# Performance work log

Hardware: AMD Instinct MI355X
Metric: run time of the kernel (lower is better)

The kernel has to match this reference:

```python
import jax, jax.numpy as jnp
import numpy as np

B, NN, HIS, MSG = 16, 1000, 12, 64
NODE_DIM, EDGE_DIM, META_DIM = 32, 16, 128
GAT_DIM = HIS * MSG            # 768
META_IN = NODE_DIM + GAT_DIM   # 800
N = B * NN                     # 16000 total nodes
E = 128000
NEG_SLOPE = 0.2


def setup_inputs() -> dict:
    key = jax.random.key(0)
    ks = jax.random.split(key, 16)
    def glorot(k, shape):
        fan_in = shape[0]
        lim = 1.0 / np.sqrt(fan_in)
        return jax.random.uniform(k, shape, jnp.float32, -lim, lim)
    return {
        "node_feature": jax.random.normal(ks[0], (B, NN, NODE_DIM), jnp.float32),
        "edge_attr": jax.random.normal(ks[1], (E, EDGE_DIM), jnp.float32),
        "message_feature": jax.random.normal(ks[2], (B, NN, HIS, MSG), jnp.float32),
        "edge_index": jax.random.randint(ks[3], (2, E), 0, N, jnp.int64) if jax.config.jax_enable_x64 else jax.random.randint(ks[3], (2, E), 0, N, jnp.int32),
        # node_learner / edge_learner
        "W_node": glorot(ks[4], (NODE_DIM, NODE_DIM)),
        "b_node": jnp.zeros((NODE_DIM,), jnp.float32),
        "W_edge": glorot(ks[5], (EDGE_DIM, EDGE_DIM)),
        "b_edge": jnp.zeros((EDGE_DIM,), jnp.float32),
        # GATConv(768, 768, heads=1, concat=False)
        "W_gat": glorot(ks[6], (GAT_DIM, GAT_DIM)),
        "att_src": glorot(ks[7], (GAT_DIM,)) * 0.1,
        "att_dst": glorot(ks[8], (GAT_DIM,)) * 0.1,
        "b_gat": jnp.zeros((GAT_DIM,), jnp.float32),
        # GNNConv([meta_in, meta_dim], dim=edge_dim)
        "W_nbr": glorot(ks[9], (2 * META_IN + EDGE_DIM, META_DIM)),
        "b_nbr": jnp.zeros((META_DIM,), jnp.float32),
        "W_self": glorot(ks[10], (META_IN, META_DIM)),
        "b_self": jnp.zeros((META_DIM,), jnp.float32),
    }


def reference(node_feature, edge_attr, message_feature, edge_index,
              W_node, b_node, W_edge, b_edge,
              W_gat, att_src, att_dst, b_gat,
              W_nbr, b_nbr, W_self, b_self):
    src, dst = edge_index[0], edge_index[1]  # j -> i

    # node / edge learners
    nf = (node_feature @ W_node + b_node).reshape(-1, NODE_DIM)        # [N, 32]
    ea = edge_attr @ W_edge + b_edge                                   # [E, 16]
    mf = message_feature.reshape(-1, GAT_DIM)                          # [N, 768]

    # --- GATConv (1 head, concat=False, add_self_loops=True, eval: no dropout) ---
    loops = jnp.arange(N, dtype=src.dtype)
    src_sl = jnp.concatenate([src, loops])
    dst_sl = jnp.concatenate([dst, loops])
    h = mf @ W_gat                                                     # [N, 768]
    a_src = h @ att_src                                                # [N]
    a_dst = h @ att_dst                                                # [N]
    alpha = jax.nn.leaky_relu(a_src[src_sl] + a_dst[dst_sl], NEG_SLOPE)  # [E+N]
    amax = jax.ops.segment_max(alpha, dst_sl, num_segments=N)
    ex = jnp.exp(alpha - amax[dst_sl])
    denom = jax.ops.segment_sum(ex, dst_sl, num_segments=N)
    coef = ex / denom[dst_sl]
    gat_out = jax.ops.segment_sum(h[src_sl] * coef[:, None], dst_sl, num_segments=N) + b_gat

    # --- meta input + GNNConv (aggr='add', batch_norm=False) ---
    x = jnp.concatenate([gat_out, nf], axis=-1)                        # [N, 800]
    z = jnp.concatenate([x[dst], x[src], ea], axis=-1)                 # [E, 1616]
    msg = z @ W_nbr + b_nbr                                            # [E, 128]
    agg = jax.ops.segment_sum(msg, dst, num_segments=N)                # [N, 128]
    out = agg + x @ W_self + b_self                                    # [N, 128]
    return out.reshape(-1, NN, META_DIM)                               # [B, 1000, 128]
```

## Files before the change

### kernel.cpp

```cpp
#include <hip/hip_runtime.h>

#define N_NODES 16000
#define N_EDGES 128000
#define GATD 768
#define NODED 32
#define EDGED 16
#define METAIN 800
#define METAD 128
#define YCOLS 384

typedef short s16x8 __attribute__((ext_vector_type(8)));
typedef float f32x4v __attribute__((ext_vector_type(4)));

__device__ __forceinline__ unsigned short f2bf(float f){
    unsigned u = __float_as_uint(f);
    return (unsigned short)((u + 0x7fffu + ((u >> 16) & 1u)) >> 16);
}
__device__ __forceinline__ float us2f(unsigned short u){ return __uint_as_float(((unsigned)u)<<16); }

__device__ __forceinline__ void gload16(const void* g, void* l){
    __builtin_amdgcn_global_load_lds((const __attribute__((address_space(1))) void*)g,
                                     (__attribute__((address_space(3))) void*)l, 16, 0, 0);
}


__global__ __launch_bounds__(256) void conv_bf16_kernel(const float* __restrict__ in,
                                                        unsigned short* __restrict__ out, int n8){
    int i = blockIdx.x*256 + threadIdx.x;
    if (i >= n8) return;
    const float4* p = reinterpret_cast<const float4*>(in) + (size_t)i*2;
    float4 a = p[0], b = p[1];
    union { unsigned short u[8]; s16x8 v; } o;
    o.u[0]=f2bf(a.x); o.u[1]=f2bf(a.y); o.u[2]=f2bf(a.z); o.u[3]=f2bf(a.w);
    o.u[4]=f2bf(b.x); o.u[5]=f2bf(b.y); o.u[6]=f2bf(b.z); o.u[7]=f2bf(b.w);
    reinterpret_cast<s16x8*>(out)[i] = o.v;
}

__global__ __launch_bounds__(256) void wgat_t_kernel(const float* __restrict__ W_gat,
                                                     unsigned short* __restrict__ WgT){
    int idx = blockIdx.x*256 + threadIdx.x;
    int c = idx / GATD, k = idx % GATD;
    WgT[idx] = f2bf(W_gat[(size_t)k*GATD + c]);
}

__global__ __launch_bounds__(256) void wcat_t_kernel(const float* __restrict__ W_nbr,
                                                     const float* __restrict__ W_self,
                                                     unsigned short* __restrict__ WcatT){
    int idx = blockIdx.x*256 + threadIdx.x;
    int c = idx / METAIN, k = idx % METAIN;
    float v;
    if (c < 128)      v = W_nbr[(size_t)k*METAD + c];
    else if (c < 256) v = W_nbr[(size_t)(800+k)*METAD + (c-128)];
    else              v = W_self[(size_t)k*METAD + (c-256)];
    WcatT[idx] = f2bf(v);
}


__global__ __launch_bounds__(256) void ea_kernel(const float* __restrict__ edge_attr,
                                                 const float* __restrict__ W_edge,
                                                 const float* __restrict__ b_edge,
                                                 float* __restrict__ ea_lin){
    __shared__ float We[256];
    __shared__ float be[16];
    int tid = threadIdx.x;
    We[tid] = W_edge[tid];
    if (tid < 16) be[tid] = b_edge[tid];
    __syncthreads();
    int idx = blockIdx.x*256 + tid;
    int e = idx >> 4, j = idx & 15;
    const float* row = edge_attr + (size_t)e*EDGED;
    float s = be[j];
    #pragma unroll
    for (int k = 0; k < 16; ++k) s += row[k] * We[k*16 + j];
    ea_lin[idx] = s;
}

__global__ __launch_bounds__(256) void nf_kernel(const float* __restrict__ node_feature,
                                                 const float* __restrict__ W_node,
                                                 const float* __restrict__ b_node,
                                                 unsigned short* __restrict__ x_bf){
    __shared__ float Wn[1024];
    __shared__ float bn[32];
    int tid = threadIdx.x;
    for (int i = tid; i < 1024; i += 256) Wn[i] = W_node[i];
    if (tid < 32) bn[tid] = b_node[tid];
    __syncthreads();
    int idx = blockIdx.x*256 + tid;
    int n = idx >> 5, j = idx & 31;
    const float* row = node_feature + (size_t)n*NODED;
    float s = bn[j];
    #pragma unroll
    for (int k = 0; k < 32; ++k) s += row[k] * Wn[k*32 + j];
    x_bf[(size_t)n*METAIN + GATD + j] = f2bf(s);
}


__global__ __launch_bounds__(256) void deg_kernel(const int* __restrict__ dst, int* __restrict__ deg){
    int e = blockIdx.x*256 + threadIdx.x;
    atomicAdd(&deg[dst[e]], 1);
}

__global__ __launch_bounds__(1024) void scan_kernel(const int* __restrict__ deg,
                                                    int* __restrict__ rowstart,
                                                    int* __restrict__ cursor){
    __shared__ int part[1024];
    int t = threadIdx.x;
    int base = t * 16;
    int local[16];
    int s = 0;
    #pragma unroll
    for (int k = 0; k < 16; ++k){
        int idx = base + k;
        int v = (idx < N_NODES) ? deg[idx] : 0;
        local[k] = s; s += v;
    }
    part[t] = s;
    __syncthreads();
    for (int off = 1; off < 1024; off <<= 1){
        int v = 0;
        if (t >= off) v = part[t-off];
        __syncthreads();
        if (t >= off) part[t] += v;
        __syncthreads();
    }
    int excl = (t == 0) ? 0 : part[t-1];
    #pragma unroll
    for (int k = 0; k < 16; ++k){
        int idx = base + k;
        if (idx < N_NODES){ int rs = excl + local[k]; rowstart[idx] = rs; cursor[idx] = rs; }
    }
    if (t == 1023) rowstart[N_NODES] = part[1023];
}

__global__ __launch_bounds__(256) void csr_kernel(const int* __restrict__ dst,
                                                  int* __restrict__ cursor,
                                                  int* __restrict__ csr){
    int e = blockIdx.x*256 + threadIdx.x;
    int p = atomicAdd(&cursor[dst[e]], 1);
    csr[p] = e;
}


template<bool BFOUT>
__global__ __launch_bounds__(256) void mfma_gemm_kernel(const unsigned short* __restrict__ A,
                                                        const unsigned short* __restrict__ Bt,
                                                        float* __restrict__ Cf,
                                                        unsigned short* __restrict__ Cb,
                                                        int Ncols, int K){
    __shared__ __align__(16) unsigned short As[128*32];
    __shared__ __align__(16) unsigned short Bs[128*32];
    int tid = threadIdx.x;
    int wave = tid >> 6, lane = tid & 63;
    int rowBase = blockIdx.y * 128, colBase = blockIdx.x * 128;
    const unsigned short* gA = A + (size_t)(rowBase + (tid>>2))*K + (tid&3)*8;
    const unsigned short* gB = Bt + (size_t)(colBase + (tid>>2))*K + (tid&3)*8;
    char* lA = (char*)As + tid*16;
    char* lB = (char*)Bs + tid*16;
    int r0 = (wave>>1)*64, c0 = (wave&1)*64;
    int rl = lane & 15, koff = (lane>>4)*8;
    f32x4v acc[4][4] = {};
    for (int k0 = 0; k0 < K; k0 += 32){
        __syncthreads();
        gload16(gA + k0,                     lA);
        gload16(gA + (size_t)64*K + k0,      lA + 4096);
        gload16(gB + k0,                     lB);
        gload16(gB + (size_t)64*K + k0,      lB + 4096);
        __syncthreads();
        s16x8 af[4], bfr[4];
        #pragma unroll
        for (int mi = 0; mi < 4; ++mi)
            af[mi] = *reinterpret_cast<const s16x8*>(&As[(r0 + mi*16 + rl)*32 + koff]);
        #pragma unroll
        for (int ni = 0; ni < 4; ++ni)
            bfr[ni] = *reinterpret_cast<const s16x8*>(&Bs[(c0 + ni*16 + rl)*32 + koff]);
        #pragma unroll
        for (int mi = 0; mi < 4; ++mi)
            #pragma unroll
            for (int ni = 0; ni < 4; ++ni)
                acc[mi][ni] = __builtin_amdgcn_mfma_f32_16x16x32_bf16(af[mi], bfr[ni], acc[mi][ni], 0, 0, 0);
    }
    int orow = rowBase + r0 + (lane>>4)*4;
    int ocol = colBase + c0 + rl;
    #pragma unroll
    for (int mi = 0; mi < 4; ++mi)
        #pragma unroll
        for (int ni = 0; ni < 4; ++ni){
            #pragma unroll
            for (int j = 0; j < 4; ++j){
                size_t idx = (size_t)(orow + mi*16 + j)*Ncols + ocol + ni*16;
                if constexpr (BFOUT) Cb[idx] = f2bf(acc[mi][ni][j]);
                else                 Cf[idx] = acc[mi][ni][j];
            }
        }
}


__global__ __launch_bounds__(256) void attn_dots_kernel(const unsigned short* __restrict__ h_bf,
                                                        const float* __restrict__ att_src,
                                                        const float* __restrict__ att_dst,
                                                        float* __restrict__ a_src,
                                                        float* __restrict__ a_dst){
    int w = threadIdx.x >> 6, lane = threadIdx.x & 63;
    int n = blockIdx.x*4 + w;
    const unsigned short* hr = h_bf + (size_t)n*GATD;
    float s = 0.f, d = 0.f;
    #pragma unroll
    for (int c = 0; c < 3; ++c){
        int o = c*256 + lane*4;
        ushort4 v  = *reinterpret_cast<const ushort4*>(hr + o);
        float4 as4 = *reinterpret_cast<const float4*>(att_src + o);
        float4 ad4 = *reinterpret_cast<const float4*>(att_dst + o);
        float f0 = us2f(v.x), f1 = us2f(v.y), f2 = us2f(v.z), f3 = us2f(v.w);
        s += f0*as4.x + f1*as4.y + f2*as4.z + f3*as4.w;
        d += f0*ad4.x + f1*ad4.y + f2*ad4.z + f3*ad4.w;
    }
    #pragma unroll
    for (int off = 32; off; off >>= 1){ s += __shfl_xor(s, off); d += __shfl_xor(d, off); }
    if (lane == 0){ a_src[n] = s; a_dst[n] = d; }
}


__global__ __launch_bounds__(256) void gat_gather_kernel(const unsigned short* __restrict__ h_bf,
                                                         const float* __restrict__ a_src,
                                                         const float* __restrict__ a_dst,
                                                         const float* __restrict__ b_gat,
                                                         const int* __restrict__ src,
                                                         const int* __restrict__ rowstart,
                                                         const int* __restrict__ csr,
                                                         unsigned short* __restrict__ x_bf){
    int wv = threadIdx.x >> 6, lane = threadIdx.x & 63;
    int i = blockIdx.x*4 + wv;
    float adi = a_dst[i];
    float al = a_src[i] + adi;
    al = al > 0.f ? al : 0.2f*al;
    float ex_self = expf(al);
    const unsigned short* hi = h_bf + (size_t)i*GATD;
    float acc[12];
    #pragma unroll
    for (int c = 0; c < 3; ++c){
        ushort4 v = *reinterpret_cast<const ushort4*>(hi + c*256 + lane*4);
        acc[c*4+0] = ex_self*us2f(v.x); acc[c*4+1] = ex_self*us2f(v.y);
        acc[c*4+2] = ex_self*us2f(v.z); acc[c*4+3] = ex_self*us2f(v.w);
    }
    float dsum = ex_self;
    int rs = rowstart[i], re = rowstart[i+1];
    for (int p = rs; p < re; p += 64){
        int cnt = min(64, re - p);
        int sv = 0; float ev = 0.f;
        if (lane < cnt){
            int e = csr[p+lane];
            sv = src[e];
            float a = a_src[sv] + adi;
            a = a > 0.f ? a : 0.2f*a;
            ev = expf(a);
        }
        for (int j = 0; j < cnt; ++j){
            int   ss = __shfl(sv, j);
            float ww = __shfl(ev, j);
            dsum += ww;
            const unsigned short* hs = h_bf + (size_t)ss*GATD;
            #pragma unroll
            for (int c = 0; c < 3; ++c){
                ushort4 v = *reinterpret_cast<const ushort4*>(hs + c*256 + lane*4);
                acc[c*4+0] += ww*us2f(v.x); acc[c*4+1] += ww*us2f(v.y);
                acc[c*4+2] += ww*us2f(v.z); acc[c*4+3] += ww*us2f(v.w);
            }
        }
    }
    float inv = 1.f / dsum;
    unsigned short* xr = x_bf + (size_t)i*METAIN;
    #pragma unroll
    for (int c = 0; c < 3; ++c){
        float4 bg = *reinterpret_cast<const float4*>(b_gat + c*256 + lane*4);
        ushort4 o;
        o.x = f2bf(acc[c*4+0]*inv + bg.x); o.y = f2bf(acc[c*4+1]*inv + bg.y);
        o.z = f2bf(acc[c*4+2]*inv + bg.z); o.w = f2bf(acc[c*4+3]*inv + bg.w);
        *reinterpret_cast<ushort4*>(xr + c*256 + lane*4) = o;
    }
}


__global__ __launch_bounds__(128) void out_gather_kernel(const float* __restrict__ y,
                                                         const float* __restrict__ ea_lin,
                                                         const float* __restrict__ W_nbr,
                                                         const float* __restrict__ b_nbr,
                                                         const float* __restrict__ b_self,
                                                         const int* __restrict__ src,
                                                         const int* __restrict__ rowstart,
                                                         const int* __restrict__ csr,
                                                         float* __restrict__ out){
    __shared__ float W3[16*128];
    __shared__ int   s_src[32];
    __shared__ int   s_eid[32];
    __shared__ float s_ea[32*16];
    int i = blockIdx.x, c = threadIdx.x;
    #pragma unroll
    for (int k = 0; k < 16; ++k) W3[k*128 + c] = W_nbr[(size_t)(1600+k)*METAD + c];
    int rs = rowstart[i], re = rowstart[i+1];
    int deg = re - rs;
    float acc = 0.f;
    for (int p = rs; p < re; p += 32){
        int cnt = min(32, re - p);
        __syncthreads();
        if (c < cnt){ int e = csr[p+c]; s_eid[c] = e; s_src[c] = src[e]; }
        __syncthreads();
        for (int idx = c; idx < cnt*16; idx += 128){
            int j = idx >> 4, k = idx & 15;
            s_ea[idx] = ea_lin[(size_t)s_eid[j]*EDGED + k];
        }
        __syncthreads();
        for (int j = 0; j < cnt; ++j){
            acc += y[(size_t)s_src[j]*YCOLS + 128 + c];
            float ez = 0.f;
            #pragma unroll
            for (int k = 0; k < 16; ++k) ez += s_ea[j*16 + k] * W3[k*128 + c];
            acc += ez;
        }
    }
    float y1 = y[(size_t)i*YCOLS + c];
    float ys = y[(size_t)i*YCOLS + 256 + c];
    float outv = (float)deg * (y1 + b_nbr[c]) + acc + ys + b_self[c];
    out[(size_t)i*METAD + c] = outv;
}


extern "C" void kernel_launch(void* const* d_in, const int* in_sizes, int n_in,
                              void* d_out, int out_size, void* d_ws, size_t ws_size,
                              hipStream_t stream){
    const float* node_feature    = (const float*)d_in[0];
    const float* edge_attr       = (const float*)d_in[1];
    const float* message_feature = (const float*)d_in[2];
    const int*   edge_index      = (const int*)d_in[3];
    const float* W_node = (const float*)d_in[4];
    const float* b_node = (const float*)d_in[5];
    const float* W_edge = (const float*)d_in[6];
    const float* b_edge = (const float*)d_in[7];
    const float* W_gat  = (const float*)d_in[8];
    const float* att_src= (const float*)d_in[9];
    const float* att_dst= (const float*)d_in[10];
    const float* b_gat  = (const float*)d_in[11];
    const float* W_nbr  = (const float*)d_in[12];
    const float* b_nbr  = (const float*)d_in[13];
    const float* W_self = (const float*)d_in[14];
    const float* b_self = (const float*)d_in[15];
    float* out = (float*)d_out;

    char* wsb = (char*)d_ws;
    size_t off = 0;
    auto walloc = [&](size_t bytes)->void*{
        void* p = wsb + off;
        off = (off + bytes + 511) & ~(size_t)511;
        return p;
    };
    unsigned short* h_bf  = (unsigned short*)walloc((size_t)N_NODES*GATD*2);
    float* y              = (float*)walloc((size_t)N_NODES*YCOLS*4);
    float* ea_lin         = (float*)walloc((size_t)N_EDGES*EDGED*4);
    unsigned short* A_bf  = (unsigned short*)walloc((size_t)N_NODES*GATD*2);
    unsigned short* x_bf  = (unsigned short*)walloc((size_t)N_NODES*METAIN*2);
    unsigned short* WgT   = (unsigned short*)walloc((size_t)GATD*GATD*2);
    unsigned short* WcatT = (unsigned short*)walloc((size_t)YCOLS*METAIN*2);
    float* a_src  = (float*)walloc((size_t)N_NODES*4);
    float* a_dst  = (float*)walloc((size_t)N_NODES*4);
    int* deg      = (int*)walloc((size_t)N_NODES*4);
    int* rowstart = (int*)walloc((size_t)(N_NODES+1)*4);
    int* cursor   = (int*)walloc((size_t)N_NODES*4);
    int* csr      = (int*)walloc((size_t)N_EDGES*4);

    const int* src = edge_index;
    const int* dst = edge_index + N_EDGES;

    hipMemsetAsync(deg, 0, (size_t)N_NODES*4, stream);

    conv_bf16_kernel<<<(N_NODES*GATD/8 + 255)/256, 256, 0, stream>>>(message_feature, A_bf, N_NODES*GATD/8);
    wgat_t_kernel<<<(GATD*GATD)/256, 256, 0, stream>>>(W_gat, WgT);
    wcat_t_kernel<<<(YCOLS*METAIN)/256, 256, 0, stream>>>(W_nbr, W_self, WcatT);

    ea_kernel<<<(N_EDGES*EDGED)/256, 256, 0, stream>>>(edge_attr, W_edge, b_edge, ea_lin);
    nf_kernel<<<(N_NODES*NODED)/256, 256, 0, stream>>>(node_feature, W_node, b_node, x_bf);
    deg_kernel<<<N_EDGES/256, 256, 0, stream>>>(dst, deg);
    scan_kernel<<<1, 1024, 0, stream>>>(deg, rowstart, cursor);
    csr_kernel<<<N_EDGES/256, 256, 0, stream>>>(dst, cursor, csr);

    mfma_gemm_kernel<true><<<dim3(GATD/128, N_NODES/128), 256, 0, stream>>>(A_bf, WgT, nullptr, h_bf, GATD, GATD);
    attn_dots_kernel<<<N_NODES/4, 256, 0, stream>>>(h_bf, att_src, att_dst, a_src, a_dst);
    gat_gather_kernel<<<N_NODES/4, 256, 0, stream>>>(h_bf, a_src, a_dst, b_gat, src, rowstart, csr, x_bf);

    mfma_gemm_kernel<false><<<dim3(YCOLS/128, N_NODES/128), 256, 0, stream>>>(x_bf, WcatT, y, nullptr, YCOLS, METAIN);
    out_gather_kernel<<<N_NODES, 128, 0, stream>>>(y, ea_lin, W_nbr, b_nbr, b_self, src, rowstart, csr, out);
}
```

Baseline: 320.4 us.

## Fuse bf16 conversion and attention dots into GAT GEMM, fold edge linear into weights

The GAT GEMM now reads fp32 message features directly and converts them to bf16 while staging into LDS. Its epilogue computes the attention dot products with shuffles and atomics, which removes the separate conversion and attn_dots passes. The edge learner is folded algebraically into the W_nbr edge block (W_edge·W3 and b_edge·W3), so the per-edge ea_lin buffer is no longer written and the gather reads raw edge_attr instead. Weight packing is merged into one kernel with a tiled transpose and the memsets are combined. The trade-offs are a non-async A load path in the GEMM and float atomics that make the a_src/a_dst summation order nondeterministic.

```diff
diff --git a/kernel.cpp b/kernel.cpp
--- a/kernel.cpp
+++ b/kernel.cpp
@@ -23,56 +23,62 @@
                                      (__attribute__((address_space(3))) void*)l, 16, 0, 0);
 }
 
-
-__global__ __launch_bounds__(256) void conv_bf16_kernel(const float* __restrict__ in,
-                                                        unsigned short* __restrict__ out, int n8){
-    int i = blockIdx.x*256 + threadIdx.x;
-    if (i >= n8) return;
-    const float4* p = reinterpret_cast<const float4*>(in) + (size_t)i*2;
-    float4 a = p[0], b = p[1];
-    union { unsigned short u[8]; s16x8 v; } o;
-    o.u[0]=f2bf(a.x); o.u[1]=f2bf(a.y); o.u[2]=f2bf(a.z); o.u[3]=f2bf(a.w);
-    o.u[4]=f2bf(b.x); o.u[5]=f2bf(b.y); o.u[6]=f2bf(b.z); o.u[7]=f2bf(b.w);
-    reinterpret_cast<s16x8*>(out)[i] = o.v;
-}
-
-__global__ __launch_bounds__(256) void wgat_t_kernel(const float* __restrict__ W_gat,
-                                                     unsigned short* __restrict__ WgT){
-    int idx = blockIdx.x*256 + threadIdx.x;
-    int c = idx / GATD, k = idx % GATD;
-    WgT[idx] = f2bf(W_gat[(size_t)k*GATD + c]);
-}
-
-__global__ __launch_bounds__(256) void wcat_t_kernel(const float* __restrict__ W_nbr,
-                                                     const float* __restrict__ W_self,
-                                                     unsigned short* __restrict__ WcatT){
-    int idx = blockIdx.x*256 + threadIdx.x;
-    int c = idx / METAIN, k = idx % METAIN;
-    float v;
-    if (c < 128)      v = W_nbr[(size_t)k*METAD + c];
-    else if (c < 256) v = W_nbr[(size_t)(800+k)*METAD + (c-128)];
-    else              v = W_self[(size_t)k*METAD + (c-256)];
-    WcatT[idx] = f2bf(v);
-}
-
-
-__global__ __launch_bounds__(256) void ea_kernel(const float* __restrict__ edge_attr,
-                                                 const float* __restrict__ W_edge,
-                                                 const float* __restrict__ b_edge,
-                                                 float* __restrict__ ea_lin){
-    __shared__ float We[256];
-    __shared__ float be[16];
-    int tid = threadIdx.x;
-    We[tid] = W_edge[tid];
-    if (tid < 16) be[tid] = b_edge[tid];
-    __syncthreads();
-    int idx = blockIdx.x*256 + tid;
-    int e = idx >> 4, j = idx & 15;
-    const float* row = edge_attr + (size_t)e*EDGED;
-    float s = be[j];
-    #pragma unroll
-    for (int k = 0; k < 16; ++k) s += row[k] * We[k*16 + j];
-    ea_lin[idx] = s;
+__global__ __launch_bounds__(256) void pack_all_kernel(const float* __restrict__ W_gat,
+                                                       const float* __restrict__ W_nbr,
+                                                       const float* __restrict__ W_self,
+                                                       const float* __restrict__ W_edge,
+                                                       const float* __restrict__ b_edge,
+                                                       unsigned short* __restrict__ WgT,
+                                                       unsigned short* __restrict__ WcatT,
+                                                       float* __restrict__ W16g,
+                                                       float* __restrict__ bbg){
+    int bid = blockIdx.x, tid = threadIdx.x;
+    if (bid < 144){
+        __shared__ float t[64][65];
+        int bi = bid / 12, bj = bid % 12;
+        int r16 = tid >> 4, c4 = (tid & 15) * 4;
+        #pragma unroll
+        for (int it = 0; it < 4; ++it){
+            int row = it*16 + r16;
+            float4 v = *reinterpret_cast<const float4*>(W_gat + (size_t)(bi*64+row)*GATD + bj*64 + c4);
+            t[row][c4+0]=v.x; t[row][c4+1]=v.y; t[row][c4+2]=v.z; t[row][c4+3]=v.w;
+        }
+        __syncthreads();
+        #pragma unroll
+        for (int it = 0; it < 4; ++it){
+            int row = it*16 + r16;
+            ushort4 o;
+            o.x = f2bf(t[c4+0][row]); o.y = f2bf(t[c4+1][row]);
+            o.z = f2bf(t[c4+2][row]); o.w = f2bf(t[c4+3][row]);
+            *reinterpret_cast<ushort4*>(WgT + (size_t)(bj*64+row)*GATD + bi*64 + c4) = o;
+        }
+    } else if (bid < 1344){
+        int idx = (bid-144)*256 + tid;
+        int c = idx / METAIN, k = idx % METAIN;
+        float v;
+        if (c < 128)      v = W_nbr[(size_t)k*METAD + c];
+        else if (c < 256) v = W_nbr[(size_t)(800+k)*METAD + (c-128)];
+        else              v = W_self[(size_t)k*METAD + (c-256)];
+        WcatT[idx] = f2bf(v);
+    } else {
+        int c = tid;
+        if (c < 128){
+            float w3[16];
+            #pragma unroll
+            for (int k = 0; k < 16; ++k) w3[k] = W_nbr[(size_t)(1600+k)*METAD + c];
+            #pragma unroll
+            for (int j = 0; j < 16; ++j){
+                float s = 0.f;
+                #pragma unroll
+                for (int k = 0; k < 16; ++k) s += W_edge[j*16+k] * w3[k];
+                W16g[j*128 + c] = s;
+            }
+            float bb = 0.f;
+            #pragma unroll
+            for (int k = 0; k < 16; ++k) bb += b_edge[k] * w3[k];
+            bbg[c] = bb;
+        }
+    }
 }
 
 __global__ __launch_bounds__(256) void nf_kernel(const float* __restrict__ node_feature,
@@ -141,19 +147,25 @@
 }
 
 
-template<bool BFOUT>
-__global__ __launch_bounds__(256) void mfma_gemm_kernel(const unsigned short* __restrict__ A,
+template<bool AF32, bool DOTS, bool BFOUT>
+__global__ __launch_bounds__(256) void mfma_gemm_kernel(const float* __restrict__ A32,
+                                                        const unsigned short* __restrict__ A16,
                                                         const unsigned short* __restrict__ Bt,
                                                         float* __restrict__ Cf,
                                                         unsigned short* __restrict__ Cb,
+                                                        const float* __restrict__ att_src,
+                                                        const float* __restrict__ att_dst,
+                                                        float* __restrict__ a_srcO,
+                                                        float* __restrict__ a_dstO,
                                                         int Ncols, int K){
     __shared__ __align__(16) unsigned short As[128*32];
     __shared__ __align__(16) unsigned short Bs[128*32];
     int tid = threadIdx.x;
     int wave = tid >> 6, lane = tid & 63;
     int rowBase = blockIdx.y * 128, colBase = blockIdx.x * 128;
-    const unsigned short* gA = A + (size_t)(rowBase + (tid>>2))*K + (tid&3)*8;
-    const unsigned short* gB = Bt + (size_t)(colBase + (tid>>2))*K + (tid&3)*8;
+    const float*          gA32p = AF32 ? A32 + (size_t)(rowBase + (tid>>2))*K + (tid&3)*8 : nullptr;
+    const unsigned short* gA16p = AF32 ? nullptr : A16 + (size_t)(rowBase + (tid>>2))*K + (tid&3)*8;
+    const unsigned short* gBp   = Bt + (size_t)(colBase + (tid>>2))*K + (tid&3)*8;
     char* lA = (char*)As + tid*16;
     char* lB = (char*)Bs + tid*16;
     int r0 = (wave>>1)*64, c0 = (wave&1)*64;
@@ -161,10 +173,24 @@
     f32x4v acc[4][4] = {};
     for (int k0 = 0; k0 < K; k0 += 32){
         __syncthreads();
-        gload16(gA + k0,                     lA);
-        gload16(gA + (size_t)64*K + k0,      lA + 4096);
-        gload16(gB + k0,                     lB);
-        gload16(gB + (size_t)64*K + k0,      lB + 4096);
+        gload16(gBp + k0,                  lB);
+        gload16(gBp + (size_t)64*K + k0,   lB + 4096);
+        if constexpr (AF32){
+            float4 a0 = *reinterpret_cast<const float4*>(gA32p + k0);
+            float4 a1 = *reinterpret_cast<const float4*>(gA32p + k0 + 4);
+            float4 a2 = *reinterpret_cast<const float4*>(gA32p + (size_t)64*K + k0);
+            float4 a3 = *reinterpret_cast<const float4*>(gA32p + (size_t)64*K + k0 + 4);
+            union { unsigned short u[8]; s16x8 v; } p0, p1;
+            p0.u[0]=f2bf(a0.x); p0.u[1]=f2bf(a0.y); p0.u[2]=f2bf(a0.z); p0.u[3]=f2bf(a0.w);
+            p0.u[4]=f2bf(a1.x); p0.u[5]=f2bf(a1.y); p0.u[6]=f2bf(a1.z); p0.u[7]=f2bf(a1.w);
+            p1.u[0]=f2bf(a2.x); p1.u[1]=f2bf(a2.y); p1.u[2]=f2bf(a2.z); p1.u[3]=f2bf(a2.w);
+            p1.u[4]=f2bf(a3.x); p1.u[5]=f2bf(a3.y); p1.u[6]=f2bf(a3.z); p1.u[7]=f2bf(a3.w);
+            *reinterpret_cast<s16x8*>(lA)        = p0.v;
+            *reinterpret_cast<s16x8*>(lA + 4096) = p1.v;
+        } else {
+            gload16(gA16p + k0,                lA);
+            gload16(gA16p + (size_t)64*K + k0, lA + 4096);
+        }
         __syncthreads();
         s16x8 af[4], bfr[4];
         #pragma unroll
@@ -192,31 +218,37 @@
                 else                 Cf[idx] = acc[mi][ni][j];
             }
         }
-}
-
-
-__global__ __launch_bounds__(256) void attn_dots_kernel(const unsigned short* __restrict__ h_bf,
-                                                        const float* __restrict__ att_src,
-                                                        const float* __restrict__ att_dst,
-                                                        float* __restrict__ a_src,
-                                                        float* __restrict__ a_dst){
-    int w = threadIdx.x >> 6, lane = threadIdx.x & 63;
-    int n = blockIdx.x*4 + w;
-    const unsigned short* hr = h_bf + (size_t)n*GATD;
-    float s = 0.f, d = 0.f;
-    #pragma unroll
-    for (int c = 0; c < 3; ++c){
-        int o = c*256 + lane*4;
-        ushort4 v  = *reinterpret_cast<const ushort4*>(hr + o);
-        float4 as4 = *reinterpret_cast<const float4*>(att_src + o);
-        float4 ad4 = *reinterpret_cast<const float4*>(att_dst + o);
-        float f0 = us2f(v.x), f1 = us2f(v.y), f2 = us2f(v.z), f3 = us2f(v.w);
-        s += f0*as4.x + f1*as4.y + f2*as4.z + f3*as4.w;
-        d += f0*ad4.x + f1*ad4.y + f2*ad4.z + f3*ad4.w;
-    }
-    #pragma unroll
-    for (int off = 32; off; off >>= 1){ s += __shfl_xor(s, off); d += __shfl_xor(d, off); }
-    if (lane == 0){ a_src[n] = s; a_dst[n] = d; }
+    if constexpr (DOTS){
+        float as_c[4], ad_c[4];
+        #pragma unroll
+        for (int ni = 0; ni < 4; ++ni){
+            int col = colBase + c0 + ni*16 + rl;
+            as_c[ni] = att_src[col];
+            ad_c[ni] = att_dst[col];
+        }
+        #pragma unroll
+        for (int mi = 0; mi < 4; ++mi)
+            #pragma unroll
+            for (int j = 0; j < 4; ++j){
+                float ps = 0.f, pd = 0.f;
+                #pragma unroll
+                for (int ni = 0; ni < 4; ++ni){
+                    float v = acc[mi][ni][j];
+                    ps += v * as_c[ni];
+                    pd += v * ad_c[ni];
+                }
+                #pragma unroll
+                for (int off = 8; off; off >>= 1){
+                    ps += __shfl_xor(ps, off);
+                    pd += __shfl_xor(pd, off);
+                }
+                if (rl == 0){
+                    int r = rowBase + r0 + mi*16 + (lane>>4)*4 + j;
+                    atomicAdd(&a_srcO[r], ps);
+                    atomicAdd(&a_dstO[r], pd);
+                }
+            }
+    }
 }
 
 
@@ -281,8 +313,9 @@
 
 
 __global__ __launch_bounds__(128) void out_gather_kernel(const float* __restrict__ y,
-                                                         const float* __restrict__ ea_lin,
-                                                         const float* __restrict__ W_nbr,
+                                                         const float* __restrict__ edge_attr,
+                                                         const float* __restrict__ W16g,
+                                                         const float* __restrict__ bbg,
                                                          const float* __restrict__ b_nbr,
                                                          const float* __restrict__ b_self,
                                                          const int* __restrict__ src,
@@ -295,7 +328,7 @@
     __shared__ float s_ea[32*16];
     int i = blockIdx.x, c = threadIdx.x;
     #pragma unroll
-    for (int k = 0; k < 16; ++k) W3[k*128 + c] = W_nbr[(size_t)(1600+k)*METAD + c];
+    for (int k = 0; k < 16; ++k) W3[k*128 + c] = W16g[k*128 + c];
     int rs = rowstart[i], re = rowstart[i+1];
     int deg = re - rs;
     float acc = 0.f;
@@ -306,7 +339,7 @@
         __syncthreads();
         for (int idx = c; idx < cnt*16; idx += 128){
             int j = idx >> 4, k = idx & 15;
-            s_ea[idx] = ea_lin[(size_t)s_eid[j]*EDGED + k];
+            s_ea[idx] = edge_attr[(size_t)s_eid[j]*EDGED + k];
         }
         __syncthreads();
         for (int j = 0; j < cnt; ++j){
@@ -319,7 +352,7 @@
     }
     float y1 = y[(size_t)i*YCOLS + c];
     float ys = y[(size_t)i*YCOLS + 256 + c];
-    float outv = (float)deg * (y1 + b_nbr[c]) + acc + ys + b_self[c];
+    float outv = (float)deg * (y1 + b_nbr[c] + bbg[c]) + acc + ys + b_self[c];
     out[(size_t)i*METAD + c] = outv;
 }
 
@@ -354,14 +387,15 @@
     };
     unsigned short* h_bf  = (unsigned short*)walloc((size_t)N_NODES*GATD*2);
     float* y              = (float*)walloc((size_t)N_NODES*YCOLS*4);
-    float* ea_lin         = (float*)walloc((size_t)N_EDGES*EDGED*4);
-    unsigned short* A_bf  = (unsigned short*)walloc((size_t)N_NODES*GATD*2);
     unsigned short* x_bf  = (unsigned short*)walloc((size_t)N_NODES*METAIN*2);
     unsigned short* WgT   = (unsigned short*)walloc((size_t)GATD*GATD*2);
     unsigned short* WcatT = (unsigned short*)walloc((size_t)YCOLS*METAIN*2);
-    float* a_src  = (float*)walloc((size_t)N_NODES*4);
-    float* a_dst  = (float*)walloc((size_t)N_NODES*4);
-    int* deg      = (int*)walloc((size_t)N_NODES*4);
+    float* W16g   = (float*)walloc(16*128*4);
+    float* bbg    = (float*)walloc(128*4);
+    float* zbase  = (float*)walloc((size_t)3*N_NODES*4);
+    float* a_src  = zbase;
+    float* a_dst  = zbase + N_NODES;
+    int*   deg    = (int*)(zbase + 2*N_NODES);
     int* rowstart = (int*)walloc((size_t)(N_NODES+1)*4);
     int* cursor   = (int*)walloc((size_t)N_NODES*4);
     int* csr      = (int*)walloc((size_t)N_EDGES*4);
@@ -369,22 +403,23 @@
     const int* src = edge_index;
     const int* dst = edge_index + N_EDGES;
 
-    hipMemsetAsync(deg, 0, (size_t)N_NODES*4, stream);
-
-    conv_bf16_kernel<<<(N_NODES*GATD/8 + 255)/256, 256, 0, stream>>>(message_feature, A_bf, N_NODES*GATD/8);
-    wgat_t_kernel<<<(GATD*GATD)/256, 256, 0, stream>>>(W_gat, WgT);
-    wcat_t_kernel<<<(YCOLS*METAIN)/256, 256, 0, stream>>>(W_nbr, W_self, WcatT);
-
-    ea_kernel<<<(N_EDGES*EDGED)/256, 256, 0, stream>>>(edge_attr, W_edge, b_edge, ea_lin);
+    hipMemsetAsync(zbase, 0, (size_t)3*N_NODES*4, stream);
+
+    pack_all_kernel<<<1345, 256, 0, stream>>>(W_gat, W_nbr, W_self, W_edge, b_edge,
+                                              WgT, WcatT, W16g, bbg);
     nf_kernel<<<(N_NODES*NODED)/256, 256, 0, stream>>>(node_feature, W_node, b_node, x_bf);
     deg_kernel<<<N_EDGES/256, 256, 0, stream>>>(dst, deg);
-    scan_kernel<<<1, 1024, 0, stream>>>(deg, rowstart, cursor);
+    scan_kernel<<<1, 1024, 0, stream>>>((const int*)deg, rowstart, cursor);
     csr_kernel<<<N_EDGES/256, 256, 0, stream>>>(dst, cursor, csr);
 
-    mfma_gemm_kernel<true><<<dim3(GATD/128, N_NODES/128), 256, 0, stream>>>(A_bf, WgT, nullptr, h_bf, GATD, GATD);
-    attn_dots_kernel<<<N_NODES/4, 256, 0, stream>>>(h_bf, att_src, att_dst, a_src, a_dst);
+    mfma_gemm_kernel<true,true,true><<<dim3(GATD/128, N_NODES/128), 256, 0, stream>>>(
+        message_feature, nullptr, WgT, nullptr, h_bf, att_src, att_dst, a_src, a_dst, GATD, GATD);
+
     gat_gather_kernel<<<N_NODES/4, 256, 0, stream>>>(h_bf, a_src, a_dst, b_gat, src, rowstart, csr, x_bf);
 
-    mfma_gemm_kernel<false><<<dim3(YCOLS/128, N_NODES/128), 256, 0, stream>>>(x_bf, WcatT, y, nullptr, YCOLS, METAIN);
-    out_gather_kernel<<<N_NODES, 128, 0, stream>>>(y, ea_lin, W_nbr, b_nbr, b_self, src, rowstart, csr, out);
-}
+    mfma_gemm_kernel<false,false,false><<<dim3(YCOLS/128, N_NODES/128), 256, 0, stream>>>(
+        nullptr, x_bf, WcatT, y, nullptr, nullptr, nullptr, nullptr, nullptr, YCOLS, METAIN);
+
+    out_gather_kernel<<<N_NODES, 128, 0, stream>>>(y, edge_attr, W16g, bbg, b_nbr, b_self,
+                                                   src, rowstart, csr, out);
+}
```

Result: faster. 311.3 us (-2.8%).
